# Kernel optimization log

Hardware: AMD Instinct MI355X
Metric: run time of the kernel (lower is better)

The kernel has to match this reference:

```python
import jax, jax.numpy as jnp
import numpy as np

V, E, H, N, B, T_CAP = 10000, 2048, 512, 98, 32, 61


def setup_inputs() -> dict:
    key = jax.random.key(0)
    ks = jax.random.split(key, 24)
    p = lambda k, shape: jax.random.normal(k, shape, dtype=jnp.float32) * 0.02
    inp = {
        "img_features": jax.random.normal(ks[0], (B, N, E), dtype=jnp.float32),
        "captions": jax.random.randint(ks[1], (B, T_CAP), 0, V),
        "emb": p(ks[2], (V, H)),
        "W_init_h": p(ks[3], (H, E)), "b_init_h": jnp.zeros((H,), jnp.float32),
        "W_init_c": p(ks[4], (H, E)), "b_init_c": jnp.zeros((H,), jnp.float32),
        "W_U": p(ks[5], (H, H)), "b_U": jnp.zeros((H,), jnp.float32),
        "W_att": p(ks[6], (H, E)), "b_att": jnp.zeros((H,), jnp.float32),
        "W_v": p(ks[7], (1, H)), "b_v": jnp.zeros((1,), jnp.float32),
        "W_fb": p(ks[8], (E, H)), "b_fb": jnp.zeros((E,), jnp.float32),
        "W_ih": p(ks[9], (4 * H, H + E)), "b_ih": jnp.zeros((4 * H,), jnp.float32),
        "W_hh": p(ks[10], (4 * H, H)), "b_hh": jnp.zeros((4 * H,), jnp.float32),
        "W_out": p(ks[11], (V, H)), "b_out": jnp.zeros((V,), jnp.float32),
    }
    return inp


def reference(img_features, captions, emb, W_init_h, b_init_h, W_init_c, b_init_c,
              W_U, b_U, W_att, b_att, W_v, b_v, W_fb, b_fb,
              W_ih, b_ih, W_hh, b_hh, W_out, b_out):
    # training-mode forward: max_timespan = caption_len - 1; dropout as identity (eval-style determinism)
    T = captions.shape[1] - 1
    avg = img_features.mean(axis=1)  # [B, E]
    h = jnp.tanh(avg @ W_init_h.T + b_init_h)  # [B, H]
    c = jnp.tanh(avg @ W_init_c.T + b_init_c)
    # Embeddings with sqrt(d_model) scaling
    emb_seq = emb[captions] * jnp.sqrt(jnp.float32(emb.shape[1]))  # [B, T_cap, H]
    # W_s is timestep-invariant: hoist out of loop (same math)
    Ws = jnp.einsum('bne,he->bnh', img_features, W_att) + b_att  # [B, N, H]

    def step(carry, emb_t):
        h, c = carry
        att = jnp.tanh(Ws + (h @ W_U.T + b_U)[:, None, :])       # [B, N, H]
        e = jnp.einsum('bnh,h->bn', att, W_v[0]) + b_v[0]        # [B, N]
        alpha = jax.nn.softmax(e, axis=1)
        context = jnp.einsum('bne,bn->be', img_features, alpha)  # [B, E]
        gate = jax.nn.sigmoid(h @ W_fb.T + b_fb)                 # [B, E]
        x = jnp.concatenate([emb_t, gate * context], axis=1)     # [B, H+E]
        gates = x @ W_ih.T + b_ih + h @ W_hh.T + b_hh            # [B, 4H]
        i_, f_, g_, o_ = jnp.split(gates, 4, axis=1)             # torch LSTMCell gate order
        c2 = jax.nn.sigmoid(f_) * c + jax.nn.sigmoid(i_) * jnp.tanh(g_)
        h2 = jax.nn.sigmoid(o_) * jnp.tanh(c2)
        pred = h2 @ W_out.T + b_out                              # [B, V]
        return (h2, c2), pred

    emb_steps = jnp.swapaxes(emb_seq[:, :T], 0, 1)  # [T, B, H]
    (_, _), preds = jax.lax.scan(step, (h, c), emb_steps)
    return jnp.swapaxes(preds, 0, 1)  # [B, T, V]
```

## Files before the change

kernel.cpp:

```cpp
#include <hip/hip_runtime.h>
#include <hip/hip_bf16.h>

#define BB   32
#define NN   98
#define EE   2048
#define HH   512
#define VV   10000
#define TT   60
#define TCAP 61

typedef unsigned short u16;
typedef __attribute__((ext_vector_type(8))) short bh8;
typedef __attribute__((ext_vector_type(4))) float f32x4;

__device__ __forceinline__ float bsf(unsigned s) {
    union { unsigned u; float f; } w; w.u = s << 16; return w.f;
}
__device__ __forceinline__ u16 f2bu(float f) {
    union { float f; unsigned u; } v; v.f = f;
    unsigned u = v.u;
    u = u + 0x7fffu + ((u >> 16) & 1u);
    return (u16)(u >> 16);
}
__device__ __forceinline__ bh8 ld8(const u16* p) {
    return *reinterpret_cast<const bh8*>(p);
}
__device__ __forceinline__ float sigm(float x) {
    return __builtin_amdgcn_rcpf(1.0f + exp2f(-1.4426950408889634f * x));
}
__device__ __forceinline__ float tanh_(float x) {
    return 1.0f - 2.0f * __builtin_amdgcn_rcpf(1.0f + exp2f(2.885390081777927f * x));
}

__global__ __launch_bounds__(256) void k_conv(
    const float* __restrict__ src, u16* __restrict__ dst)
{
    int i = blockIdx.x * 256 + threadIdx.x;
    float4 v = reinterpret_cast<const float4*>(src)[i];
    ushort4 o;
    o.x = f2bu(v.x); o.y = f2bu(v.y); o.z = f2bu(v.z); o.w = f2bu(v.w);
    reinterpret_cast<ushort4*>(dst)[i] = o;
}

__global__ __launch_bounds__(256) void k_init1(
    const float* __restrict__ img, const int* __restrict__ caps,
    const float* __restrict__ emb, u16* __restrict__ avg_bf, u16* __restrict__ emb_all)
{
    int bid = blockIdx.x, tid = threadIdx.x;
    if (bid < 256) {
        int b = bid >> 3, et = bid & 7;
        int ec = et * 256 + tid;
        const float* p = img + (size_t)(b * NN) * EE + ec;
        float s = 0.f;
        for (int n = 0; n < NN; ++n) s += p[(size_t)n * EE];
        avg_bf[b * EE + ec] = f2bu(s * (1.0f / 98.0f));
    } else {
        int eb = bid - 256;
        for (int r8 = 0; r8 < 8; ++r8) {
            int row = eb * 8 + r8;
            int t = row >> 5, b = row & 31;
            int cap = caps[b * TCAP + t];
            const float* src = emb + (size_t)cap * HH;
            u16* dst = emb_all + (size_t)row * HH;
            for (int c = tid; c < HH; c += 256)
                dst[c] = f2bu(src[c] * 22.627416997969522f);
        }
    }
}

__global__ __launch_bounds__(256) void k_init2(
    const u16* __restrict__ avg_bf,
    const u16* __restrict__ Wh_bf, const float* __restrict__ b_h,
    const u16* __restrict__ Wc_bf, const float* __restrict__ b_c,
    u16* __restrict__ h_all, float* __restrict__ c_ws)
{
    __shared__ float red[4][2][64][4];
    int ot = blockIdx.x, tid = threadIdx.x;
    int w = tid >> 6, lane = tid & 63, quad = lane >> 4, l16 = lane & 15;
    int o = ot * 16 + l16;
    const u16* wrow = (o < HH) ? (Wh_bf + (size_t)o * EE) : (Wc_bf + (size_t)(o - HH) * EE);
    f32x4 acc[2]; acc[0] = {0,0,0,0}; acc[1] = {0,0,0,0};
    for (int c = w * 16; c < w * 16 + 16; ++c) {
        int k = c * 32 + quad * 8;
        bh8 b8 = ld8(wrow + k);
        for (int mt = 0; mt < 2; ++mt) {
            bh8 a8 = ld8(avg_bf + (size_t)(mt * 16 + l16) * EE + k);
            acc[mt] = __builtin_amdgcn_mfma_f32_16x16x32_bf16(a8, b8, acc[mt], 0, 0, 0);
        }
    }
    for (int mt = 0; mt < 2; ++mt)
        for (int r = 0; r < 4; ++r) red[w][mt][lane][r] = acc[mt][r];
    __syncthreads();
    for (int idx = tid; idx < 512; idx += 256) {
        int mg = idx >> 4, nn2 = idx & 15;
        int mt = mg >> 4, m = mg & 15;
        int sl = nn2 + 16 * (m >> 2), rg = m & 3;
        float v = red[0][mt][sl][rg] + red[1][mt][sl][rg] + red[2][mt][sl][rg] + red[3][mt][sl][rg];
        int oo = ot * 16 + nn2, b = mg;
        if (oo < HH)
            h_all[(size_t)b * HH + oo] = f2bu(tanh_(v + b_h[oo]));
        else
            c_ws[b * HH + (oo - HH)] = tanh_(v + b_c[oo - HH]);
    }
}

__global__ __launch_bounds__(256) void k_ws(
    const u16* __restrict__ img_bf, const u16* __restrict__ Watt_bf,
    const float* __restrict__ b_att, u16* __restrict__ Ws_bf)
{
    int bid = blockIdx.x, tid = threadIdx.x;
    int mt = bid >> 4, nt = bid & 15;
    int w = tid >> 6, lane = tid & 63, quad = lane >> 4, l16 = lane & 15;
    int rowA = mt * 64 + w * 16 + l16;
    f32x4 acc[2]; acc[0] = {0,0,0,0}; acc[1] = {0,0,0,0};
    const u16* arow = img_bf + (size_t)rowA * EE;
    for (int c = 0; c < 64; ++c) {
        int k = c * 32 + quad * 8;
        bh8 a8 = ld8(arow + k);
        for (int s = 0; s < 2; ++s) {
            bh8 b8 = ld8(Watt_bf + (size_t)(nt * 32 + s * 16 + l16) * EE + k);
            acc[s] = __builtin_amdgcn_mfma_f32_16x16x32_bf16(a8, b8, acc[s], 0, 0, 0);
        }
    }
    for (int s = 0; s < 2; ++s)
        for (int r = 0; r < 4; ++r) {
            int m = quad * 4 + r;
            int row = mt * 64 + w * 16 + m;
            int col = nt * 32 + s * 16 + l16;
            Ws_bf[(size_t)row * HH + col] = f2bu(acc[s][r] + b_att[col]);
        }
}

__global__ __launch_bounds__(256) void k_c(
    const u16* __restrict__ h_all, int tIn,
    const u16* __restrict__ WU_bf, const float* __restrict__ b_U,
    const u16* __restrict__ Wfb_bf, const float* __restrict__ b_fb,
    float* __restrict__ Wu_ws, float* __restrict__ gate_ws)
{
    __shared__ float red[4][2][64][4];
    int ot = blockIdx.x, tid = threadIdx.x;
    int w = tid >> 6, lane = tid & 63, quad = lane >> 4, l16 = lane & 15;
    int o = ot * 16 + l16;
    const u16* wrow = (o < HH) ? (WU_bf + (size_t)o * HH) : (Wfb_bf + (size_t)(o - HH) * HH);
    const u16* hbase = h_all + (size_t)tIn * BB * HH;
    f32x4 acc[2]; acc[0] = {0,0,0,0}; acc[1] = {0,0,0,0};
    for (int c = w * 4; c < w * 4 + 4; ++c) {
        int k = c * 32 + quad * 8;
        bh8 b8 = ld8(wrow + k);
        for (int mt = 0; mt < 2; ++mt) {
            bh8 a8 = ld8(hbase + (size_t)(mt * 16 + l16) * HH + k);
            acc[mt] = __builtin_amdgcn_mfma_f32_16x16x32_bf16(a8, b8, acc[mt], 0, 0, 0);
        }
    }
    for (int mt = 0; mt < 2; ++mt)
        for (int r = 0; r < 4; ++r) red[w][mt][lane][r] = acc[mt][r];
    __syncthreads();
    for (int idx = tid; idx < 512; idx += 256) {
        int mg = idx >> 4, nn2 = idx & 15;
        int mt = mg >> 4, m = mg & 15;
        int sl = nn2 + 16 * (m >> 2), rg = m & 3;
        float v = red[0][mt][sl][rg] + red[1][mt][sl][rg] + red[2][mt][sl][rg] + red[3][mt][sl][rg];
        int oo = ot * 16 + nn2, b = mg;
        if (oo < HH)
            Wu_ws[b * HH + oo] = v + b_U[oo];
        else
            gate_ws[b * EE + (oo - HH)] = sigm(v + b_fb[oo - HH]);
    }
}

__global__ __launch_bounds__(256) void k_a(
    const float* __restrict__ img, const u16* __restrict__ Ws_bf,
    const float* __restrict__ Wu_ws, const float* __restrict__ gate_ws,
    const float* __restrict__ W_v, const float* __restrict__ b_v,
    u16* __restrict__ xctx)
{
    __shared__ float e_sh[NN];
    __shared__ float a_sh[NN];
    int bid = blockIdx.x, tid = threadIdx.x;
    int b = bid >> 2, et = bid & 3;
    int w = tid >> 6, lane = tid & 63;
    float wu[8], wv[8];
    {
        const float* wup = Wu_ws + b * HH + lane * 8;
        const float* wvp = W_v + lane * 8;
        #pragma unroll
        for (int j = 0; j < 8; ++j) { wu[j] = wup[j]; wv[j] = wvp[j]; }
    }
    for (int n = w; n < NN; n += 4) {
        bh8 ws8 = ld8(Ws_bf + (size_t)(b * NN + n) * HH + lane * 8);
        float acc = 0.f;
        #pragma unroll
        for (int j = 0; j < 8; ++j) acc += wv[j] * tanh_(bsf((u16)ws8[j]) + wu[j]);
        #pragma unroll
        for (int off = 32; off > 0; off >>= 1) acc += __shfl_down(acc, off, 64);
        if (lane == 0) e_sh[n] = acc + b_v[0];
    }
    __syncthreads();
    if (tid < 64) {
        float e0 = e_sh[tid];
        float e1 = (tid + 64 < NN) ? e_sh[tid + 64] : -1e30f;
        float m = fmaxf(e0, e1);
        #pragma unroll
        for (int off = 32; off > 0; off >>= 1) m = fmaxf(m, __shfl_xor(m, off, 64));
        const float L2E = 1.4426950408889634f;
        float x0 = exp2f((e0 - m) * L2E);
        float x1 = (tid + 64 < NN) ? exp2f((e1 - m) * L2E) : 0.f;
        float s = x0 + x1;
        #pragma unroll
        for (int off = 32; off > 0; off >>= 1) s += __shfl_xor(s, off, 64);
        float inv = __builtin_amdgcn_rcpf(s);
        a_sh[tid] = x0 * inv;
        if (tid + 64 < NN) a_sh[tid + 64] = x1 * inv;
    }
    __syncthreads();
    int ec = et * 512 + tid * 2;
    const float* ip = img + (size_t)b * NN * EE + ec;
    float c0 = 0.f, c1 = 0.f;
    for (int n = 0; n < NN; ++n) {
        float2 u = *reinterpret_cast<const float2*>(ip + (size_t)n * EE);
        float a = a_sh[n];
        c0 = fmaf(a, u.x, c0); c1 = fmaf(a, u.y, c1);
    }
    float g0 = gate_ws[b * EE + ec], g1 = gate_ws[b * EE + ec + 1];
    unsigned outw = ((unsigned)f2bu(g1 * c1) << 16) | (unsigned)f2bu(g0 * c0);
    *reinterpret_cast<unsigned*>(xctx + (size_t)b * EE + ec) = outw;
}

__global__ __launch_bounds__(256) void k_b(
    int t,
    const u16* __restrict__ emb_all, const u16* __restrict__ xctx,
    u16* h_all,
    const u16* __restrict__ Wih_bf, const float* __restrict__ b_ih,
    const u16* __restrict__ Whh_bf, const float* __restrict__ b_hh,
    float* __restrict__ c_ws)
{
    __shared__ float red[4][64][4];
    __shared__ float gsh[16][16];
    int bid = blockIdx.x, tid = threadIdx.x;
    int kt = bid & 127, mt = bid >> 7;
    int w = tid >> 6, lane = tid & 63, quad = lane >> 4, l16 = lane & 15;
    int brow = mt * 16 + l16;
    int j = kt * 4 + (l16 & 3) + HH * (l16 >> 2);
    const u16* embrow = emb_all + (size_t)(t * BB + brow) * HH;
    const u16* xrow   = xctx + (size_t)brow * EE;
    const u16* hrow   = h_all + (size_t)(t * BB + brow) * HH;
    const u16* wih    = Wih_bf + (size_t)j * (HH + EE);
    const u16* whh    = Whh_bf + (size_t)j * HH;
    f32x4 acc = {0,0,0,0};
    for (int c = w * 24; c < w * 24 + 24; ++c) {
        int k = c * 32 + quad * 8;
        bh8 a8, b8;
        if (c < 16)      a8 = ld8(embrow + k);
        else if (c < 80) a8 = ld8(xrow + (k - HH));
        else             a8 = ld8(hrow + (k - HH - EE));
        if (c < 80)      b8 = ld8(wih + k);
        else             b8 = ld8(whh + (k - HH - EE));
        acc = __builtin_amdgcn_mfma_f32_16x16x32_bf16(a8, b8, acc, 0, 0, 0);
    }
    for (int r = 0; r < 4; ++r) red[w][lane][r] = acc[r];
    __syncthreads();
    {
        int m = tid >> 4, nn2 = tid & 15;
        int sl = nn2 + 16 * (m >> 2), rg = m & 3;
        int jj = kt * 4 + (nn2 & 3) + HH * (nn2 >> 2);
        float v = red[0][sl][rg] + red[1][sl][rg] + red[2][sl][rg] + red[3][sl][rg]
                + b_ih[jj] + b_hh[jj];
        gsh[m][nn2] = v;
    }
    __syncthreads();
    if (tid < 64) {
        int m = tid >> 2, i = tid & 3;
        int b = mt * 16 + m, k = kt * 4 + i;
        float gi = gsh[m][i], gf = gsh[m][i + 4], gg = gsh[m][i + 8], go = gsh[m][i + 12];
        float cold = c_ws[b * HH + k];
        float c2 = sigm(gf) * cold + sigm(gi) * tanh_(gg);
        float h2 = sigm(go) * tanh_(c2);
        c_ws[b * HH + k] = c2;
        h_all[(size_t)((t + 1) * BB + b) * HH + k] = f2bu(h2);
    }
}

__global__ __launch_bounds__(256) void k_pred(
    const u16* __restrict__ h_all, const u16* __restrict__ Wout_bf,
    const float* __restrict__ b_out, float* __restrict__ out)
{
    int bid = blockIdx.x, tid = threadIdx.x;
    int mt = bid / 79, vt = bid % 79;
    int w = tid >> 6, lane = tid & 63, quad = lane >> 4, l16 = lane & 15;
    f32x4 acc[8][2];
    for (int mi = 0; mi < 8; ++mi) for (int s = 0; s < 2; ++s) acc[mi][s] = {0,0,0,0};
    int nact[2]; int vbase[2];
    for (int s = 0; s < 2; ++s) {
        int ntg = vt * 8 + 2 * w + s;
        nact[s] = (ntg < 625);
        vbase[s] = ntg * 16;
    }
    for (int c = 0; c < 16; ++c) {
        int k = c * 32 + quad * 8;
        bh8 b8[2];
        for (int s = 0; s < 2; ++s) if (nact[s])
            b8[s] = ld8(Wout_bf + (size_t)(vbase[s] + l16) * HH + k);
        for (int mi = 0; mi < 8; ++mi) {
            int row = 32 + mt * 128 + mi * 16 + l16;
            bh8 a8 = ld8(h_all + (size_t)row * HH + k);
            for (int s = 0; s < 2; ++s) if (nact[s])
                acc[mi][s] = __builtin_amdgcn_mfma_f32_16x16x32_bf16(a8, b8[s], acc[mi][s], 0, 0, 0);
        }
    }
    for (int s = 0; s < 2; ++s) if (nact[s]) {
        int v = vbase[s] + l16;
        float bo = b_out[v];
        for (int mi = 0; mi < 8; ++mi)
            for (int r = 0; r < 4; ++r) {
                int row = 32 + mt * 128 + mi * 16 + quad * 4 + r;
                int tt = (row >> 5) - 1, b = row & 31;
                out[(size_t)(b * TT + tt) * VV + v] = acc[mi][s][r] + bo;
            }
    }
}

extern "C" void kernel_launch(void* const* d_in, const int* in_sizes, int n_in,
                              void* d_out, int out_size, void* d_ws, size_t ws_size,
                              hipStream_t stream)
{
    const float* img      = (const float*)d_in[0];
    const int*   caps     = (const int*)d_in[1];
    const float* emb      = (const float*)d_in[2];
    const float* W_init_h = (const float*)d_in[3];
    const float* b_init_h = (const float*)d_in[4];
    const float* W_init_c = (const float*)d_in[5];
    const float* b_init_c = (const float*)d_in[6];
    const float* W_U      = (const float*)d_in[7];
    const float* b_U      = (const float*)d_in[8];
    const float* W_att    = (const float*)d_in[9];
    const float* b_att    = (const float*)d_in[10];
    const float* W_v      = (const float*)d_in[11];
    const float* b_v      = (const float*)d_in[12];
    const float* W_fb     = (const float*)d_in[13];
    const float* b_fb     = (const float*)d_in[14];
    const float* W_ih     = (const float*)d_in[15];
    const float* b_ih     = (const float*)d_in[16];
    const float* W_hh     = (const float*)d_in[17];
    const float* b_hh     = (const float*)d_in[18];
    const float* W_out    = (const float*)d_in[19];
    const float* b_out    = (const float*)d_in[20];
    float* out = (float*)d_out;

    char* ws = (char*)d_ws;
    u16*   img_bf  = (u16*)(ws);
    u16*   Watt_bf = (u16*)(ws + 12845056);
    u16*   Winh_bf = (u16*)(ws + 14942208);
    u16*   Winc_bf = (u16*)(ws + 17039360);
    u16*   WU_bf   = (u16*)(ws + 19136512);
    u16*   Wfb_bf  = (u16*)(ws + 19660800);
    u16*   Wih_bf  = (u16*)(ws + 21757952);
    u16*   Whh_bf  = (u16*)(ws + 32243712);
    u16*   Wout_bf = (u16*)(ws + 34340864);
    u16*   Ws_bf   = (u16*)(ws + 44580864);
    u16*   emb_all = (u16*)(ws + 47792128);
    u16*   h_all   = (u16*)(ws + 49758208);
    u16*   xctx    = (u16*)(ws + 51757056);
    u16*   avg_bf  = (u16*)(ws + 51888128);
    float* c_ws    = (float*)(ws + 52019200);
    float* Wu_ws   = (float*)(ws + 52084736);
    float* gate_ws = (float*)(ws + 52150272);

    k_conv<<<6272, 256, 0, stream>>>(img,      img_bf);
    k_conv<<<1024, 256, 0, stream>>>(W_att,    Watt_bf);
    k_conv<<<1024, 256, 0, stream>>>(W_init_h, Winh_bf);
    k_conv<<<1024, 256, 0, stream>>>(W_init_c, Winc_bf);
    k_conv<<< 256, 256, 0, stream>>>(W_U,      WU_bf);
    k_conv<<<1024, 256, 0, stream>>>(W_fb,     Wfb_bf);
    k_conv<<<5120, 256, 0, stream>>>(W_ih,     Wih_bf);
    k_conv<<<1024, 256, 0, stream>>>(W_hh,     Whh_bf);
    k_conv<<<5000, 256, 0, stream>>>(W_out,    Wout_bf);

    k_init1<<<496, 256, 0, stream>>>(img, caps, emb, avg_bf, emb_all);
    k_init2<<<64, 256, 0, stream>>>(avg_bf, Winh_bf, b_init_h, Winc_bf, b_init_c, h_all, c_ws);
    k_ws<<<784, 256, 0, stream>>>(img_bf, Watt_bf, b_att, Ws_bf);
    k_c<<<160, 256, 0, stream>>>(h_all, 0, WU_bf, b_U, Wfb_bf, b_fb, Wu_ws, gate_ws);
    for (int t = 0; t < TT; ++t) {
        k_a<<<128, 256, 0, stream>>>(img, Ws_bf, Wu_ws, gate_ws, W_v, b_v, xctx);
        k_b<<<256, 256, 0, stream>>>(t, emb_all, xctx, h_all, Wih_bf, b_ih, Whh_bf, b_hh, c_ws);
        if (t < TT - 1)
            k_c<<<160, 256, 0, stream>>>(h_all, t + 1, WU_bf, b_U, Wfb_bf, b_fb, Wu_ws, gate_ws);
    }
    k_pred<<<1185, 256, 0, stream>>>(h_all, Wout_bf, b_out, out);
}
```

Baseline: 2.688 ms.

## Fuse per-timestep recurrent kernels into one persistent kernel with grid barriers

Replaces the 179 separate per-timestep launches of k_c, k_a and k_b with a single persistent 256-block kernel. Inside it, phases are separated by software grid barriers built on an atomic counter in global memory. The attention context now reads the bf16 copy of the image features instead of fp32, halving those loads. Prediction outputs use nontemporal stores. This removes launch overhead and inter-kernel gaps, but depends on all 256 blocks being co-resident and adds atomic spin and fence cost at every barrier.

```diff
diff --git a/kernel.cpp b/kernel.cpp
--- a/kernel.cpp
+++ b/kernel.cpp
@@ -8,6 +8,7 @@
 #define VV   10000
 #define TT   60
 #define TCAP 61
+#define GG   256
 
 typedef unsigned short u16;
 typedef __attribute__((ext_vector_type(8))) short bh8;
@@ -30,6 +31,22 @@
 }
 __device__ __forceinline__ float tanh_(float x) {
     return 1.0f - 2.0f * __builtin_amdgcn_rcpf(1.0f + exp2f(2.885390081777927f * x));
+}
+
+__device__ __forceinline__ void gbar(unsigned* bar, unsigned target) {
+    __threadfence();
+    __syncthreads();
+    if (threadIdx.x == 0) {
+        atomicAdd(bar, 1u);
+        while (__hip_atomic_load(bar, __ATOMIC_RELAXED, __HIP_MEMORY_SCOPE_AGENT) < target)
+            __builtin_amdgcn_s_sleep(1);
+    }
+    __syncthreads();
+    __threadfence();
+}
+
+__global__ __launch_bounds__(64) void k_zero(unsigned* bar) {
+    if (threadIdx.x == 0) *bar = 0u;
 }
 
 __global__ __launch_bounds__(256) void k_conv(
@@ -131,18 +148,17 @@
         }
 }
 
-__global__ __launch_bounds__(256) void k_c(
-    const u16* __restrict__ h_all, int tIn,
-    const u16* __restrict__ WU_bf, const float* __restrict__ b_U,
+
+__device__ __forceinline__ void phaseA(float* sm, int g, int t,
+    const u16* h_all, const u16* __restrict__ WU_bf, const float* __restrict__ b_U,
     const u16* __restrict__ Wfb_bf, const float* __restrict__ b_fb,
-    float* __restrict__ Wu_ws, float* __restrict__ gate_ws)
-{
-    __shared__ float red[4][2][64][4];
-    int ot = blockIdx.x, tid = threadIdx.x;
+    float* Wu_ws, float* gate_ws)
+{
+    int tid = threadIdx.x;
     int w = tid >> 6, lane = tid & 63, quad = lane >> 4, l16 = lane & 15;
-    int o = ot * 16 + l16;
+    int o = g * 16 + l16;
     const u16* wrow = (o < HH) ? (WU_bf + (size_t)o * HH) : (Wfb_bf + (size_t)(o - HH) * HH);
-    const u16* hbase = h_all + (size_t)tIn * BB * HH;
+    const u16* hbase = h_all + (size_t)t * BB * HH;
     f32x4 acc[2]; acc[0] = {0,0,0,0}; acc[1] = {0,0,0,0};
     for (int c = w * 4; c < w * 4 + 4; ++c) {
         int k = c * 32 + quad * 8;
@@ -153,14 +169,18 @@
         }
     }
     for (int mt = 0; mt < 2; ++mt)
-        for (int r = 0; r < 4; ++r) red[w][mt][lane][r] = acc[mt][r];
+        for (int r = 0; r < 4; ++r)
+            sm[(((w * 2 + mt) * 64) + lane) * 4 + r] = acc[mt][r];
     __syncthreads();
     for (int idx = tid; idx < 512; idx += 256) {
         int mg = idx >> 4, nn2 = idx & 15;
         int mt = mg >> 4, m = mg & 15;
         int sl = nn2 + 16 * (m >> 2), rg = m & 3;
-        float v = red[0][mt][sl][rg] + red[1][mt][sl][rg] + red[2][mt][sl][rg] + red[3][mt][sl][rg];
-        int oo = ot * 16 + nn2, b = mg;
+        float v = sm[(((0 * 2 + mt) * 64) + sl) * 4 + rg]
+                + sm[(((1 * 2 + mt) * 64) + sl) * 4 + rg]
+                + sm[(((2 * 2 + mt) * 64) + sl) * 4 + rg]
+                + sm[(((3 * 2 + mt) * 64) + sl) * 4 + rg];
+        int oo = g * 16 + nn2, b = mg;
         if (oo < HH)
             Wu_ws[b * HH + oo] = v + b_U[oo];
         else
@@ -168,16 +188,16 @@
     }
 }
 
-__global__ __launch_bounds__(256) void k_a(
-    const float* __restrict__ img, const u16* __restrict__ Ws_bf,
-    const float* __restrict__ Wu_ws, const float* __restrict__ gate_ws,
+__device__ __forceinline__ void phaseB(float* sm, int g,
+    const u16* __restrict__ img_bf, const u16* __restrict__ Ws_bf,
+    const float* Wu_ws, const float* gate_ws,
     const float* __restrict__ W_v, const float* __restrict__ b_v,
-    u16* __restrict__ xctx)
-{
-    __shared__ float e_sh[NN];
-    __shared__ float a_sh[NN];
-    int bid = blockIdx.x, tid = threadIdx.x;
-    int b = bid >> 2, et = bid & 3;
+    u16* xctx)
+{
+    float* e_sh = sm;
+    float* a_sh = sm + 128;
+    int tid = threadIdx.x;
+    int b = g >> 2, et = g & 3;
     int w = tid >> 6, lane = tid & 63;
     float wu[8], wv[8];
     {
@@ -214,30 +234,29 @@
     }
     __syncthreads();
     int ec = et * 512 + tid * 2;
-    const float* ip = img + (size_t)b * NN * EE + ec;
+    const u16* ip = img_bf + (size_t)b * NN * EE + ec;
     float c0 = 0.f, c1 = 0.f;
     for (int n = 0; n < NN; ++n) {
-        float2 u = *reinterpret_cast<const float2*>(ip + (size_t)n * EE);
+        unsigned u = *reinterpret_cast<const unsigned*>(ip + (size_t)n * EE);
         float a = a_sh[n];
-        c0 = fmaf(a, u.x, c0); c1 = fmaf(a, u.y, c1);
+        c0 = fmaf(a, bsf(u & 0xffffu), c0);
+        c1 = fmaf(a, bsf(u >> 16), c1);
     }
     float g0 = gate_ws[b * EE + ec], g1 = gate_ws[b * EE + ec + 1];
     unsigned outw = ((unsigned)f2bu(g1 * c1) << 16) | (unsigned)f2bu(g0 * c0);
     *reinterpret_cast<unsigned*>(xctx + (size_t)b * EE + ec) = outw;
 }
 
-__global__ __launch_bounds__(256) void k_b(
-    int t,
-    const u16* __restrict__ emb_all, const u16* __restrict__ xctx,
-    u16* h_all,
+__device__ __forceinline__ void phaseC(float* sm, int g, int t,
+    const u16* __restrict__ emb_all, const u16* xctx, u16* h_all,
     const u16* __restrict__ Wih_bf, const float* __restrict__ b_ih,
     const u16* __restrict__ Whh_bf, const float* __restrict__ b_hh,
-    float* __restrict__ c_ws)
-{
-    __shared__ float red[4][64][4];
-    __shared__ float gsh[16][16];
-    int bid = blockIdx.x, tid = threadIdx.x;
-    int kt = bid & 127, mt = bid >> 7;
+    float* c_ws)
+{
+    float* red = sm;
+    float* gsh = sm + 1024;
+    int tid = threadIdx.x;
+    int kt = g & 127, mt = g >> 7;
     int w = tid >> 6, lane = tid & 63, quad = lane >> 4, l16 = lane & 15;
     int brow = mt * 16 + l16;
     int j = kt * 4 + (l16 & 3) + HH * (l16 >> 2);
@@ -257,26 +276,52 @@
         else             b8 = ld8(whh + (k - HH - EE));
         acc = __builtin_amdgcn_mfma_f32_16x16x32_bf16(a8, b8, acc, 0, 0, 0);
     }
-    for (int r = 0; r < 4; ++r) red[w][lane][r] = acc[r];
+    for (int r = 0; r < 4; ++r) red[(w * 64 + lane) * 4 + r] = acc[r];
     __syncthreads();
     {
         int m = tid >> 4, nn2 = tid & 15;
         int sl = nn2 + 16 * (m >> 2), rg = m & 3;
         int jj = kt * 4 + (nn2 & 3) + HH * (nn2 >> 2);
-        float v = red[0][sl][rg] + red[1][sl][rg] + red[2][sl][rg] + red[3][sl][rg]
+        float v = red[(0 * 64 + sl) * 4 + rg] + red[(1 * 64 + sl) * 4 + rg]
+                + red[(2 * 64 + sl) * 4 + rg] + red[(3 * 64 + sl) * 4 + rg]
                 + b_ih[jj] + b_hh[jj];
-        gsh[m][nn2] = v;
+        gsh[m * 16 + nn2] = v;
     }
     __syncthreads();
     if (tid < 64) {
         int m = tid >> 2, i = tid & 3;
         int b = mt * 16 + m, k = kt * 4 + i;
-        float gi = gsh[m][i], gf = gsh[m][i + 4], gg = gsh[m][i + 8], go = gsh[m][i + 12];
+        float gi = gsh[m * 16 + i], gf = gsh[m * 16 + i + 4];
+        float gg = gsh[m * 16 + i + 8], go = gsh[m * 16 + i + 12];
         float cold = c_ws[b * HH + k];
         float c2 = sigm(gf) * cold + sigm(gi) * tanh_(gg);
         float h2 = sigm(go) * tanh_(c2);
         c_ws[b * HH + k] = c2;
         h_all[(size_t)((t + 1) * BB + b) * HH + k] = f2bu(h2);
+    }
+}
+
+__global__ __launch_bounds__(256) void k_mega(
+    const u16* __restrict__ img_bf, const u16* __restrict__ Ws_bf,
+    const u16* __restrict__ emb_all,
+    u16* h_all, float* c_ws, float* Wu_ws, float* gate_ws, u16* xctx,
+    const u16* __restrict__ WU_bf, const float* __restrict__ b_U,
+    const u16* __restrict__ Wfb_bf, const float* __restrict__ b_fb,
+    const float* __restrict__ W_v, const float* __restrict__ b_v,
+    const u16* __restrict__ Wih_bf, const float* __restrict__ b_ih,
+    const u16* __restrict__ Whh_bf, const float* __restrict__ b_hh,
+    unsigned* bar)
+{
+    __shared__ float sm[2048];
+    int g = blockIdx.x;
+    unsigned tgt = 0;
+    for (int t = 0; t < TT; ++t) {
+        if (g < 160) phaseA(sm, g, t, h_all, WU_bf, b_U, Wfb_bf, b_fb, Wu_ws, gate_ws);
+        tgt += GG; gbar(bar, tgt);
+        if (g < 128) phaseB(sm, g, img_bf, Ws_bf, Wu_ws, gate_ws, W_v, b_v, xctx);
+        tgt += GG; gbar(bar, tgt);
+        phaseC(sm, g, t, emb_all, xctx, h_all, Wih_bf, b_ih, Whh_bf, b_hh, c_ws);
+        if (t < TT - 1) { tgt += GG; gbar(bar, tgt); }
     }
 }
 
@@ -314,7 +359,8 @@
             for (int r = 0; r < 4; ++r) {
                 int row = 32 + mt * 128 + mi * 16 + quad * 4 + r;
                 int tt = (row >> 5) - 1, b = row & 31;
-                out[(size_t)(b * TT + tt) * VV + v] = acc[mi][s][r] + bo;
+                __builtin_nontemporal_store(acc[mi][s][r] + bo,
+                                            &out[(size_t)(b * TT + tt) * VV + v]);
             }
     }
 }
@@ -364,6 +410,7 @@
     float* c_ws    = (float*)(ws + 52019200);
     float* Wu_ws   = (float*)(ws + 52084736);
     float* gate_ws = (float*)(ws + 52150272);
+    unsigned* bar  = (unsigned*)(ws + 52412416);
 
     k_conv<<<6272, 256, 0, stream>>>(img,      img_bf);
     k_conv<<<1024, 256, 0, stream>>>(W_att,    Watt_bf);
@@ -374,16 +421,16 @@
     k_conv<<<5120, 256, 0, stream>>>(W_ih,     Wih_bf);
     k_conv<<<1024, 256, 0, stream>>>(W_hh,     Whh_bf);
     k_conv<<<5000, 256, 0, stream>>>(W_out,    Wout_bf);
+    k_zero<<<1, 64, 0, stream>>>(bar);
 
     k_init1<<<496, 256, 0, stream>>>(img, caps, emb, avg_bf, emb_all);
     k_init2<<<64, 256, 0, stream>>>(avg_bf, Winh_bf, b_init_h, Winc_bf, b_init_c, h_all, c_ws);
     k_ws<<<784, 256, 0, stream>>>(img_bf, Watt_bf, b_att, Ws_bf);
-    k_c<<<160, 256, 0, stream>>>(h_all, 0, WU_bf, b_U, Wfb_bf, b_fb, Wu_ws, gate_ws);
-    for (int t = 0; t < TT; ++t) {
-        k_a<<<128, 256, 0, stream>>>(img, Ws_bf, Wu_ws, gate_ws, W_v, b_v, xctx);
-        k_b<<<256, 256, 0, stream>>>(t, emb_all, xctx, h_all, Wih_bf, b_ih, Whh_bf, b_hh, c_ws);
-        if (t < TT - 1)
-            k_c<<<160, 256, 0, stream>>>(h_all, t + 1, WU_bf, b_U, Wfb_bf, b_fb, Wu_ws, gate_ws);
-    }
+
+    k_mega<<<GG, 256, 0, stream>>>(img_bf, Ws_bf, emb_all,
+                                   h_all, c_ws, Wu_ws, gate_ws, xctx,
+                                   WU_bf, b_U, Wfb_bf, b_fb, W_v, b_v,
+                                   Wih_bf, b_ih, Whh_bf, b_hh, bar);
+
     k_pred<<<1185, 256, 0, stream>>>(h_all, Wout_bf, b_out, out);
 }
```

Measured after the change: 10.45 ms. 3.89x slower.
